# Kernel tuning notes

Hardware: AMD Instinct MI355X
Metric: run time of the kernel (lower is better)

Reference implementation:

```python
import jax, jax.numpy as jnp
import numpy as np

N_NODES = 100000

def _sage(x, src, tgt, Wl, bl, Wr):
    # PyG SAGEConv (mean aggr): out = lin_l(mean_{j in N(i)} x_j) + lin_r(x_i)
    msg = x[src]                                             # [E, F] gather
    s = jax.ops.segment_sum(msg, tgt, num_segments=N_NODES)  # [N, F]
    cnt = jax.ops.segment_sum(jnp.ones((src.shape[0], 1), x.dtype), tgt, num_segments=N_NODES)
    agg = s / jnp.maximum(cnt, 1.0)
    return agg @ Wl + bl + x @ Wr


def setup_inputs() -> dict:
    key = jax.random.key(0)
    ks = jax.random.split(key, 16)
    node_dim, edge_dim, hidden = 128, 16, 64
    E = 1000000
    x = jax.random.normal(ks[0], (N_NODES, node_dim), jnp.float32)
    edge_index = jax.random.randint(ks[1], (2, E), 0, N_NODES, jnp.int64)
    edge_attr = jax.random.normal(ks[2], (E, edge_dim), jnp.float32)
    def lin(k, fi, fo, scale=None):
        s = scale if scale is not None else 1.0 / np.sqrt(fi)
        return jax.random.uniform(k, (fi, fo), jnp.float32, -s, s)
    return {
        "x": x, "edge_index": edge_index, "edge_attr": edge_attr,
        # edge MLP: Linear(16,64) -> ReLU -> Linear(64,64)
        "We1": lin(ks[3], edge_dim, hidden), "be1": jnp.zeros((hidden,), jnp.float32),
        "We2": lin(ks[4], hidden, hidden),   "be2": jnp.zeros((hidden,), jnp.float32),
        # SAGEConv 0: lin_l (with bias, on aggregated) + lin_r (no bias, on root)
        "Wl0": lin(ks[5], node_dim, hidden), "bl0": jnp.zeros((hidden,), jnp.float32),
        "Wr0": lin(ks[6], node_dim, hidden),
        # SAGEConv 1
        "Wl1": lin(ks[7], hidden, hidden), "bl1": jnp.zeros((hidden,), jnp.float32),
        "Wr1": lin(ks[8], hidden, hidden),
        # output MLP: Linear(64,64) -> ReLU -> (Dropout eval=id) -> Linear(64,1)
        "Wo1": lin(ks[9], hidden, hidden), "bo1": jnp.zeros((hidden,), jnp.float32),
        "Wo2": lin(ks[10], hidden, 1),     "bo2": jnp.zeros((1,), jnp.float32),
    }


def reference(x, edge_index, edge_attr, We1, be1, We2, be2,
              Wl0, bl0, Wr0, Wl1, bl1, Wr1, Wo1, bo1, Wo2, bo2):
    src, tgt = edge_index[0], edge_index[1]
    # edge MLP (dropout in eval mode = identity)
    ea = jax.nn.relu(edge_attr @ We1 + be1) @ We2 + be2       # [E, H]
    # two SAGE layers with ReLU
    h = jax.nn.relu(_sage(x, src, tgt, Wl0, bl0, Wr0))        # [N, H]
    h = jax.nn.relu(_sage(h, src, tgt, Wl1, bl1, Wr1))        # [N, H]
    # per-edge features: gather both endpoints + edge embedding
    ef = h[src] + h[tgt] + ea                                 # [E, H]
    out = jax.nn.relu(ef @ Wo1 + bo1) @ Wo2 + bo2             # [E, 1]
    return jax.nn.sigmoid(out[:, 0])                          # [E]
```

## Files before the change

kernel.cpp:

```cpp
#include <hip/hip_runtime.h>
#include <math.h>

typedef __attribute__((ext_vector_type(8))) short short8;
typedef __attribute__((ext_vector_type(4))) float f32x4;

#define CAPB 4096

static __device__ __forceinline__ unsigned short f2bf(float f) {
  union { float f; unsigned int u; } x; x.f = f;
  unsigned int r = x.u + 0x7fffu + ((x.u >> 16) & 1u);
  return (unsigned short)(r >> 16);
}
static __device__ __forceinline__ float bf2f(unsigned int u) {
  union { unsigned int u; float f; } x; x.u = u << 16; return x.f;
}

__global__ void k_flag(const unsigned int* __restrict__ w, int nSample,
                       unsigned int* __restrict__ flag,
                       int* __restrict__ gcursor) {
  if (blockIdx.x == 1) {
    if (threadIdx.x < 256) { gcursor[threadIdx.x] = 0; gcursor[threadIdx.x + 256] = 0; }
    return;
  }
  if (blockIdx.x != 0) return;
  __shared__ unsigned int red[256];
  unsigned int v = 0;
  for (int i = threadIdx.x; i < nSample; i += 256) v |= w[2 * i + 1];
  red[threadIdx.x] = v;
  __syncthreads();
  for (int s = 128; s > 0; s >>= 1) {
    if (threadIdx.x < s) red[threadIdx.x] |= red[threadIdx.x + s];
    __syncthreads();
  }
  if (threadIdx.x == 0) flag[0] = red[0];
}

template <int K, bool BF16IN, int NTILES, bool INLINEW>
__device__ __forceinline__ void ngemm_body(
    const void* __restrict__ Xv, const unsigned short* __restrict__ WnT,
    const float* __restrict__ W0f, const float* __restrict__ W1f,
    unsigned short* __restrict__ Y0, unsigned short* __restrict__ Y1,
    int N, int blk, unsigned short* __restrict__ sX) {
  constexpr int STR = K + 8;
  constexpr int NC = K / 32;
  const int tid = threadIdx.x;
  const int wv = tid >> 6, lane = tid & 63;
  const int m = lane & 15, q = lane >> 4;
  const int row0 = blk * 64;

  short8 bB[NTILES][NC];
#pragma unroll
  for (int ct = 0; ct < NTILES; ++ct)
#pragma unroll
    for (int c = 0; c < NC; ++c) {
      if constexpr (INLINEW) {
        int n = (NTILES == 2) ? (wv * 32 + ct * 16 + m) : (wv * 16 + m);
        const float* Wf = (n < 64) ? W0f : W1f;
        int nn = n & 63;
        union { short8 s; unsigned short h[8]; } ub;
#pragma unroll
        for (int j = 0; j < 8; ++j)
          ub.h[j] = f2bf(Wf[(size_t)(c * 32 + q * 8 + j) * 64 + nn]);
        bB[ct][c] = ub.s;
      } else {
        int n = (NTILES == 2) ? (wv * 32 + ct * 16 + m) : (wv * 16 + m);
        bB[ct][c] = *(const short8*)(WnT + (size_t)n * K + c * 32 + q * 8);
      }
    }

#pragma unroll
  for (int i = 0; i < K / 16; ++i) {
    int f = tid + 256 * i;
    int r = f / (K / 4);
    int c4 = f % (K / 4);
    int rr = row0 + r; if (rr >= N) rr = N - 1;
    uint2 pk;
    if constexpr (BF16IN) {
      pk = *(const uint2*)((const unsigned short*)Xv + (size_t)rr * K + c4 * 4);
    } else {
      float4 v = *(const float4*)((const float*)Xv + (size_t)rr * K + c4 * 4);
      pk.x = (unsigned int)f2bf(v.x) | ((unsigned int)f2bf(v.y) << 16);
      pk.y = (unsigned int)f2bf(v.z) | ((unsigned int)f2bf(v.w) << 16);
    }
    *(uint2*)(sX + r * STR + c4 * 4) = pk;
  }
  __syncthreads();

  f32x4 acc[4][NTILES];
#pragma unroll
  for (int rt = 0; rt < 4; ++rt)
#pragma unroll
    for (int ct = 0; ct < NTILES; ++ct)
#pragma unroll
      for (int r = 0; r < 4; ++r) acc[rt][ct][r] = 0.f;

#pragma unroll
  for (int c = 0; c < NC; ++c) {
    short8 a[4];
#pragma unroll
    for (int rt = 0; rt < 4; ++rt)
      a[rt] = *(const short8*)(sX + (rt * 16 + m) * STR + c * 32 + q * 8);
#pragma unroll
    for (int rt = 0; rt < 4; ++rt)
#pragma unroll
      for (int ct = 0; ct < NTILES; ++ct)
        acc[rt][ct] = __builtin_amdgcn_mfma_f32_16x16x32_bf16(a[rt], bB[ct][c], acc[rt][ct], 0, 0, 0);
  }

#pragma unroll
  for (int rt = 0; rt < 4; ++rt)
#pragma unroll
    for (int ct = 0; ct < NTILES; ++ct) {
      unsigned short* Yw;
      int n;
      if constexpr (NTILES == 2) {
        Yw = (wv < 2) ? Y0 : Y1;
        n = (wv & 1) * 32 + ct * 16 + m;
      } else {
        Yw = Y0;
        n = wv * 16 + m;
      }
#pragma unroll
      for (int reg = 0; reg < 4; ++reg) {
        int row = row0 + rt * 16 + q * 4 + reg;
        if (row < N) Yw[(size_t)row * 64 + n] = f2bf(acc[rt][ct][reg]);
      }
    }
}

template <int K, bool BF16IN, int NTILES>
__global__ __launch_bounds__(256) void k_ngemm(
    const void* __restrict__ Xv, const unsigned short* __restrict__ WnT,
    unsigned short* __restrict__ Y0, unsigned short* __restrict__ Y1, int N) {
  __shared__ __align__(16) unsigned short sX[64 * (K + 8)];
  ngemm_body<K, BF16IN, NTILES, false>(Xv, WnT, nullptr, nullptr, Y0, Y1, N,
                                       blockIdx.x, sX);
}

__global__ __launch_bounds__(256) void k_mega1(
    const unsigned int* __restrict__ w, const unsigned int* __restrict__ flag,
    int E, int nDec, int nWork, int gB, int nConvThreads,
    int* __restrict__ src, int* __restrict__ tgt,
    int* __restrict__ gcursor, unsigned int* __restrict__ tmp,
    const float* __restrict__ x, unsigned short* __restrict__ Yl,
    unsigned short* __restrict__ Yr, int N,
    const float* __restrict__ We2, const float* __restrict__ Wo1,
    const float* __restrict__ be2, const float* __restrict__ bo1,
    const float* __restrict__ We1,
    const float* __restrict__ Wl0, const float* __restrict__ Wr0,
    const float* __restrict__ Wl1, const float* __restrict__ Wr1,
    unsigned short* __restrict__ W25T, unsigned short* __restrict__ We1T,
    unsigned short* __restrict__ Wo1T, float* __restrict__ cvec,
    unsigned short* __restrict__ WnT1,
    const float4* __restrict__ ef, uint2* __restrict__ eb) {
  __shared__ __align__(16) char smem[64 * 136 * 2];
  const int tid = threadIdx.x;
  const int tot = nDec + nWork;
  const int di  = (int)(((long long)blockIdx.x * nDec) / tot);
  const int di1 = (int)(((long long)(blockIdx.x + 1) * nDec) / tot);

  if (di1 > di) {
    int* hist = (int*)smem;
    hist[tid] = 0; hist[tid + 256] = 0;
    __syncthreads();
    const int e0 = di * 4096;
    const int e1 = (e0 + 4096 < E) ? (e0 + 4096) : E;
    const unsigned int fl = flag[0];
    for (int e = e0 + tid; e < e1; e += 256) {
      int s, t;
      if (fl) { s = (int)w[e]; t = (int)w[E + e]; }
      else    { s = (int)w[2 * e]; t = (int)w[2 * (E + e)]; }
      src[e] = s; tgt[e] = t;
      atomicAdd(hist + (t >> 8), 1);
    }
    __syncthreads();
    {
      int c0 = hist[tid], c1 = hist[tid + 256];
      int s0 = (c0 > 0) ? atomicAdd(gcursor + tid, c0) : 0;
      int s1 = (c1 > 0) ? atomicAdd(gcursor + tid + 256, c1) : 0;
      __syncthreads();
      hist[tid] = s0; hist[tid + 256] = s1;
    }
    __syncthreads();
    for (int e = e0 + tid; e < e1; e += 256) {
      int s, t;
      if (fl) { s = (int)w[e]; t = (int)w[E + e]; }
      else    { s = (int)w[2 * e]; t = (int)w[2 * (E + e)]; }
      int b = t >> 8;
      int pos = atomicAdd(hist + b, 1);
      if (pos < CAPB)
        tmp[(size_t)b * CAPB + pos] = ((unsigned int)s << 8) | (unsigned int)(t & 255);
    }
    return;
  }
  const int wi = blockIdx.x - di;
  if (wi == 0) {
    float* sB = (float*)smem;
    for (int i = tid; i < 1024; i += 256)
      *(float4*)&sB[i * 4] = *(const float4*)(Wo1 + i * 4);
    __syncthreads();
    for (int idx = tid; idx < 4096; idx += 256) {
      int k = idx >> 6, n = idx & 63;
      float s = 0.f;
#pragma unroll 8
      for (int mm = 0; mm < 64; ++mm) s = fmaf(We2[k * 64 + mm], sB[mm * 64 + n], s);
      W25T[n * 64 + k] = f2bf(s);
      Wo1T[n * 64 + k] = f2bf(sB[k * 64 + n]);
    }
    for (int idx = tid; idx < 2048; idx += 256) {
      int n = idx >> 5, k = idx & 31;
      We1T[n * 32 + k] = (k < 16) ? f2bf(We1[k * 64 + n]) : (unsigned short)0;
    }
    if (tid < 64) {
      float s = bo1[tid];
#pragma unroll 8
      for (int mm = 0; mm < 64; ++mm) s = fmaf(be2[mm], sB[mm * 64 + tid], s);
      cvec[tid] = s;
    }
  } else if (wi <= 32) {
    int idx = (wi - 1) * 256 + tid;
    int n = idx >> 6, k = idx & 63;
    float v = (n < 64) ? Wl1[(size_t)k * 64 + n] : Wr1[(size_t)k * 64 + (n - 64)];
    WnT1[idx] = f2bf(v);
  } else if (wi < 33 + gB) {
    ngemm_body<128, false, 2, true>(x, nullptr, Wl0, Wr0, Yl, Yr, N,
                                    wi - 33, (unsigned short*)smem);
  } else {
    int gid = (wi - 33 - gB) * 256 + tid;
    int nItems = E * 4;
    for (int i = gid; i < nItems; i += nConvThreads) {
      float4 v = ef[i];
      uint2 pk;
      pk.x = (unsigned int)f2bf(v.x) | ((unsigned int)f2bf(v.y) << 16);
      pk.y = (unsigned int)f2bf(v.z) | ((unsigned int)f2bf(v.w) << 16);
      eb[i] = pk;
    }
  }
}

__global__ __launch_bounds__(256) void k_bsort(
    const unsigned int* __restrict__ tmp, const int* __restrict__ gcursor,
    int* __restrict__ csrc, uint2* __restrict__ rowptr2, int N) {
  __shared__ int cnt[256];
  __shared__ int curs[256];
  __shared__ int wsum[4];
  const int b = blockIdx.x, tid = threadIdx.x;
  int c = gcursor[b]; if (c > CAPB) c = CAPB;
  cnt[tid] = 0;
  __syncthreads();
  const unsigned int* reg = tmp + (size_t)b * CAPB;
  for (int i = tid; i < c; i += 256) atomicAdd(&cnt[reg[i] & 255u], 1);
  __syncthreads();
  const int lane = tid & 63, wv = tid >> 6;
  int v = cnt[tid];
  int incl = v;
#pragma unroll
  for (int off = 1; off < 64; off <<= 1) {
    int t = __shfl_up(incl, off, 64);
    if (lane >= off) incl += t;
  }
  if (lane == 63) wsum[wv] = incl;
  __syncthreads();
  int add = 0;
  for (int ww = 0; ww < wv; ++ww) add += wsum[ww];
  int excl = add + incl - v;
  curs[tid] = excl;
  int node = b * 256 + tid;
  if (node < N)
    rowptr2[node] = make_uint2((unsigned int)(b * CAPB + excl),
                               (unsigned int)(b * CAPB + excl + v));
  __syncthreads();
  for (int i = tid; i < c; i += 256) {
    unsigned int wd = reg[i];
    int p = atomicAdd(&curs[wd & 255u], 1);
    csrc[(size_t)b * CAPB + p] = (int)(wd >> 8);
  }
}

__global__ __launch_bounds__(256) void k_agg(
    const unsigned short* __restrict__ Y, const uint2* __restrict__ rowptr2,
    const int* __restrict__ csrc, const float* __restrict__ bias,
    const unsigned short* __restrict__ Yr, unsigned short* __restrict__ H,
    int N) {
  int node = (blockIdx.x * 256 + threadIdx.x) >> 6;
  if (node >= N) return;
  const int lane = threadIdx.x & 63;
  const int c4 = lane & 15, rr = lane >> 4;
  uint2 be = rowptr2[node];
  int beg = (int)be.x, end = (int)be.y;
  float a0 = 0.f, a1 = 0.f, a2 = 0.f, a3 = 0.f;
  float b0 = 0.f, b1 = 0.f, b2 = 0.f, b3 = 0.f;
  for (int e = beg; e < end; e += 8) {
    int e0 = e + rr, e1 = e + 4 + rr;
    if (e0 < end) {
      int s = csrc[e0];
      uint2 v = *(const uint2*)(Y + (size_t)s * 64 + c4 * 4);
      a0 += bf2f(v.x & 0xffffu); a1 += bf2f(v.x >> 16);
      a2 += bf2f(v.y & 0xffffu); a3 += bf2f(v.y >> 16);
    }
    if (e1 < end) {
      int s = csrc[e1];
      uint2 v = *(const uint2*)(Y + (size_t)s * 64 + c4 * 4);
      b0 += bf2f(v.x & 0xffffu); b1 += bf2f(v.x >> 16);
      b2 += bf2f(v.y & 0xffffu); b3 += bf2f(v.y >> 16);
    }
  }
  a0 += b0; a1 += b1; a2 += b2; a3 += b3;
#pragma unroll
  for (int msk = 16; msk <= 32; msk <<= 1) {
    a0 += __shfl_xor(a0, msk, 64);
    a1 += __shfl_xor(a1, msk, 64);
    a2 += __shfl_xor(a2, msk, 64);
    a3 += __shfl_xor(a3, msk, 64);
  }
  if (rr == 0) {
    float cdeg = (float)(end - beg);
    if (cdeg < 1.f) cdeg = 1.f;
    float inv = 1.f / cdeg;
    float4 bv = *(const float4*)(bias + c4 * 4);
    uint2 yv = *(const uint2*)(Yr + (size_t)node * 64 + c4 * 4);
    float o0 = fmaxf(a0 * inv + bv.x + bf2f(yv.x & 0xffffu), 0.f);
    float o1 = fmaxf(a1 * inv + bv.y + bf2f(yv.x >> 16), 0.f);
    float o2 = fmaxf(a2 * inv + bv.z + bf2f(yv.y & 0xffffu), 0.f);
    float o3 = fmaxf(a3 * inv + bv.w + bf2f(yv.y >> 16), 0.f);
    uint2 pk;
    pk.x = (unsigned int)f2bf(o0) | ((unsigned int)f2bf(o1) << 16);
    pk.y = (unsigned int)f2bf(o2) | ((unsigned int)f2bf(o3) << 16);
    *(uint2*)(H + (size_t)node * 64 + c4 * 4) = pk;
  }
}

#define T1_STRIDE 72
#define G_STRIDE 68
__global__ __launch_bounds__(256) void k_edge3(
    const unsigned short* __restrict__ EAb, const int* __restrict__ src,
    const int* __restrict__ tgt, const unsigned short* __restrict__ Gb,
    const unsigned short* __restrict__ We1T,
    const unsigned short* __restrict__ W25T,
    const float* __restrict__ cvec, const float* __restrict__ be1,
    const float* __restrict__ Wo2, const float* __restrict__ bo2,
    float* __restrict__ out, int E, int nT, int nWaves) {
  __shared__ unsigned short sT1a[4][16 * T1_STRIDE];
  __shared__ float sGa[4][16 * G_STRIDE];
  const int tid = threadIdx.x;
  const int wid = tid >> 6, lane = tid & 63;
  const int m = lane & 15, q = lane >> 4;
  unsigned short* sT1 = sT1a[wid];
  float* sG = sGa[wid];

  short8 bWe1[4], bW25[4][2];
  float cv[4], wo2v[4], be1v[4];
#pragma unroll
  for (int nt = 0; nt < 4; ++nt) {
    int n = nt * 16 + m;
    bWe1[nt] = *(const short8*)(We1T + n * 32 + q * 8);
    bW25[nt][0] = *(const short8*)(W25T + n * 64 + q * 8);
    bW25[nt][1] = *(const short8*)(W25T + n * 64 + 32 + q * 8);
    cv[nt] = cvec[n];
    wo2v[nt] = Wo2[n];
    be1v[nt] = be1[n];
  }
  const float b_out = bo2[0];
  const short8 zfrag = {};

  int t = blockIdx.x * 4 + wid;
  if (t >= nT) return;
  int il = t * 16 + m; if (il >= E) il = E - 1;
  int my_idx = (lane < 16) ? src[il] : ((lane < 32) ? tgt[il] : 0);

  while (true) {
    const int base = t * 16;
    const int tn = t + nWaves;
    const bool last = (tn >= nT);
    const int tc = last ? t : tn;

    int il_n = tc * 16 + m; if (il_n >= E) il_n = E - 1;
    int idx_n = (lane < 16) ? src[il_n] : ((lane < 32) ? tgt[il_n] : 0);

    int rs[4], rt[4];
#pragma unroll
    for (int r = 0; r < 4; ++r) {
      rs[r] = __shfl(my_idx, q * 4 + r, 64);
      rt[r] = __shfl(my_idx, 16 + q * 4 + r, 64);
    }
    uint2 sv[4], tv[4];
#pragma unroll
    for (int r = 0; r < 4; ++r) {
      sv[r] = *(const uint2*)(Gb + (size_t)rs[r] * 64 + m * 4);
      tv[r] = *(const uint2*)(Gb + (size_t)rt[r] * 64 + m * 4);
    }

    int er = base + m; if (er >= E) er = E - 1;
    short8 aEA = zfrag;
    if (q < 2) aEA = *(const short8*)(EAb + (size_t)er * 16 + (q & 1) * 8);

    f32x4 t1[4];
#pragma unroll
    for (int nt = 0; nt < 4; ++nt) {
      f32x4 cinit; cinit[0] = be1v[nt]; cinit[1] = be1v[nt];
      cinit[2] = be1v[nt]; cinit[3] = be1v[nt];
      t1[nt] = __builtin_amdgcn_mfma_f32_16x16x32_bf16(aEA, bWe1[nt], cinit, 0, 0, 0);
    }
#pragma unroll
    for (int nt = 0; nt < 4; ++nt)
#pragma unroll
      for (int r = 0; r < 4; ++r)
        sT1[(q * 4 + r) * T1_STRIDE + nt * 16 + m] = f2bf(fmaxf(t1[nt][r], 0.f));
    short8 aT0 = *(short8*)(sT1 + m * T1_STRIDE + q * 8);
    short8 aT1 = *(short8*)(sT1 + m * T1_STRIDE + 32 + q * 8);

#pragma unroll
    for (int r = 0; r < 4; ++r) {
      f32x4 g;
      g[0] = bf2f(sv[r].x & 0xffffu) + bf2f(tv[r].x & 0xffffu);
      g[1] = bf2f(sv[r].x >> 16)     + bf2f(tv[r].x >> 16);
      g[2] = bf2f(sv[r].y & 0xffffu) + bf2f(tv[r].y & 0xffffu);
      g[3] = bf2f(sv[r].y >> 16)     + bf2f(tv[r].y >> 16);
      *(f32x4*)(sG + (q * 4 + r) * G_STRIDE + m * 4) = g;
    }

    f32x4 acc[4];
#pragma unroll
    for (int nt = 0; nt < 4; ++nt)
#pragma unroll
      for (int r = 0; r < 4; ++r)
        acc[nt][r] = cv[nt] + sG[(q * 4 + r) * G_STRIDE + nt * 16 + m];
#pragma unroll
    for (int nt = 0; nt < 4; ++nt) {
      acc[nt] = __builtin_amdgcn_mfma_f32_16x16x32_bf16(aT0, bW25[nt][0], acc[nt], 0, 0, 0);
      acc[nt] = __builtin_amdgcn_mfma_f32_16x16x32_bf16(aT1, bW25[nt][1], acc[nt], 0, 0, 0);
    }

    float p[4];
#pragma unroll
    for (int r = 0; r < 4; ++r) {
      p[r] = fmaxf(acc[0][r], 0.f) * wo2v[0] + fmaxf(acc[1][r], 0.f) * wo2v[1] +
             fmaxf(acc[2][r], 0.f) * wo2v[2] + fmaxf(acc[3][r], 0.f) * wo2v[3];
    }
#pragma unroll
    for (int msk = 1; msk <= 8; msk <<= 1) {
#pragma unroll
      for (int r = 0; r < 4; ++r) p[r] += __shfl_xor(p[r], msk, 64);
    }
    if (m == 0) {
#pragma unroll
      for (int r = 0; r < 4; ++r) {
        int row = base + q * 4 + r;
        if (row < E) out[row] = 1.f / (1.f + __expf(-(p[r] + b_out)));
      }
    }

    if (last) break;
    t = tn; my_idx = idx_n;
  }
}

extern "C" void kernel_launch(void* const* d_in, const int* in_sizes, int n_in,
                              void* d_out, int out_size, void* d_ws, size_t ws_size,
                              hipStream_t stream) {
  const float* x     = (const float*)d_in[0];
  const unsigned int* eidx = (const unsigned int*)d_in[1];
  const float* eattr = (const float*)d_in[2];
  const float* We1 = (const float*)d_in[3];
  const float* be1 = (const float*)d_in[4];
  const float* We2 = (const float*)d_in[5];
  const float* be2 = (const float*)d_in[6];
  const float* Wl0 = (const float*)d_in[7];
  const float* bl0 = (const float*)d_in[8];
  const float* Wr0 = (const float*)d_in[9];
  const float* Wl1 = (const float*)d_in[10];
  const float* bl1 = (const float*)d_in[11];
  const float* Wr1 = (const float*)d_in[12];
  const float* Wo1 = (const float*)d_in[13];
  const float* bo1 = (const float*)d_in[14];
  const float* Wo2 = (const float*)d_in[15];
  const float* bo2 = (const float*)d_in[16];

  const int N = in_sizes[0] / 128;
  const int E = in_sizes[2] / 16;
  const int NBUCK = (N + 255) >> 8;
  float* out = (float*)d_out;

  char* ws = (char*)d_ws;
  size_t off = 0;
  auto alloc = [&](size_t bytes) {
    char* p = ws + off;
    off += (bytes + 255) & ~(size_t)255;
    return p;
  };
  unsigned int* flag = (unsigned int*)alloc(256);
  int* src    = (int*)alloc((size_t)E * 4);
  int* tgt    = (int*)alloc((size_t)E * 4);
  int* gcursor = (int*)alloc(512 * 4);
  unsigned int* tmp = (unsigned int*)alloc((size_t)NBUCK * CAPB * 4);
  int* csrc   = (int*)alloc((size_t)NBUCK * CAPB * 4);
  uint2* rowptr2 = (uint2*)alloc((size_t)N * 8);
  unsigned short* EAb = (unsigned short*)alloc((size_t)E * 16 * 2);
  unsigned short* Hb = (unsigned short*)alloc((size_t)N * 64 * 2);
  unsigned short* Yl = (unsigned short*)alloc((size_t)N * 64 * 2);
  unsigned short* Yr = (unsigned short*)alloc((size_t)N * 64 * 2);
  unsigned short* Gb = (unsigned short*)alloc((size_t)N * 64 * 2);
  unsigned short* W25T = (unsigned short*)alloc(64 * 64 * 2);
  unsigned short* We1T = (unsigned short*)alloc(64 * 32 * 2);
  unsigned short* Wo1T = (unsigned short*)alloc(64 * 64 * 2);
  unsigned short* WnT1 = (unsigned short*)alloc(128 * 64 * 2);
  float* cvec = (float*)alloc(64 * 4);
  (void)ws_size; (void)n_in; (void)out_size;

  k_flag<<<2, 256, 0, stream>>>(eidx, 8192, flag, gcursor);

  const int nDec = (E + 4095) / 4096;
  const int gB = (N + 63) / 64;
  const int convB = 1024;
  const int nWork = 33 + gB + convB;
  k_mega1<<<nDec + nWork, 256, 0, stream>>>(
      eidx, flag, E, nDec, nWork, gB, convB * 256,
      src, tgt, gcursor, tmp,
      x, Yl, Yr, N,
      We2, Wo1, be2, bo1, We1, Wl0, Wr0, Wl1, Wr1,
      W25T, We1T, Wo1T, cvec, WnT1,
      (const float4*)eattr, (uint2*)EAb);

  k_bsort<<<NBUCK, 256, 0, stream>>>(tmp, gcursor, csrc, rowptr2, N);

  const int aggB = (N + 3) / 4;
  k_agg<<<aggB, 256, 0, stream>>>(Yl, rowptr2, csrc, bl0, Yr, Hb, N);

  k_ngemm<64, true, 2><<<gB, 256, 0, stream>>>(Hb, WnT1, Yl, Yr, N);
  k_agg<<<aggB, 256, 0, stream>>>(Yl, rowptr2, csrc, bl1, Yr, Hb, N);

  k_ngemm<64, true, 1><<<gB, 256, 0, stream>>>(Hb, Wo1T, Gb, nullptr, N);

  const int nT = (E + 15) / 16;
  const int blocks = 3072;
  k_edge3<<<blocks, 256, 0, stream>>>(EAb, src, tgt, Gb, We1T, W25T, cvec,
                                      be1, Wo2, bo2, out, E, nT, blocks * 4);
}
```

Before: 398.6 us.

## Replace global bucket cursor atomics with per-decode-block bucket slots

The edge bucketing pass no longer reserves space in each bucket with global atomicAdd on a shared cursor array. Each decode block now writes its per-bucket counts to a counts matrix and scatters into its own fixed-capacity slot region (48 entries per bucket per block). The bucket-sort kernel then scans all slots of each bucket, masked by those counts. This removes global atomic contention and the cursor reset from k_flag, at the cost of a sparser tmp layout, extra slot scanning and an integer division per slot. With one million edges over 391 buckets and 245 decode blocks, the expected per-slot load is about 16, so overflow past 48 is unlikely but would silently drop edges.

```diff
diff --git a/kernel.cpp b/kernel.cpp
--- a/kernel.cpp
+++ b/kernel.cpp
@@ -5,6 +5,8 @@
 typedef __attribute__((ext_vector_type(4))) float f32x4;
 
 #define CAPB 4096
+#define CAPPB 48
+#define NDECP 256
 
 static __device__ __forceinline__ unsigned short f2bf(float f) {
   union { float f; unsigned int u; } x; x.f = f;
@@ -16,13 +18,7 @@
 }
 
 __global__ void k_flag(const unsigned int* __restrict__ w, int nSample,
-                       unsigned int* __restrict__ flag,
-                       int* __restrict__ gcursor) {
-  if (blockIdx.x == 1) {
-    if (threadIdx.x < 256) { gcursor[threadIdx.x] = 0; gcursor[threadIdx.x + 256] = 0; }
-    return;
-  }
-  if (blockIdx.x != 0) return;
+                       unsigned int* __restrict__ flag) {
   __shared__ unsigned int red[256];
   unsigned int v = 0;
   for (int i = threadIdx.x; i < nSample; i += 256) v |= w[2 * i + 1];
@@ -141,7 +137,7 @@
     const unsigned int* __restrict__ w, const unsigned int* __restrict__ flag,
     int E, int nDec, int nWork, int gB, int nConvThreads,
     int* __restrict__ src, int* __restrict__ tgt,
-    int* __restrict__ gcursor, unsigned int* __restrict__ tmp,
+    int* __restrict__ counts, unsigned int* __restrict__ tmp,
     const float* __restrict__ x, unsigned short* __restrict__ Yl,
     unsigned short* __restrict__ Yr, int N,
     const float* __restrict__ We2, const float* __restrict__ Wo1,
@@ -176,10 +172,10 @@
     __syncthreads();
     {
       int c0 = hist[tid], c1 = hist[tid + 256];
-      int s0 = (c0 > 0) ? atomicAdd(gcursor + tid, c0) : 0;
-      int s1 = (c1 > 0) ? atomicAdd(gcursor + tid + 256, c1) : 0;
+      counts[(size_t)tid * NDECP + di] = c0;
+      counts[(size_t)(tid + 256) * NDECP + di] = c1;
       __syncthreads();
-      hist[tid] = s0; hist[tid + 256] = s1;
+      hist[tid] = 0; hist[tid + 256] = 0;
     }
     __syncthreads();
     for (int e = e0 + tid; e < e1; e += 256) {
@@ -188,8 +184,9 @@
       else    { s = (int)w[2 * e]; t = (int)w[2 * (E + e)]; }
       int b = t >> 8;
       int pos = atomicAdd(hist + b, 1);
-      if (pos < CAPB)
-        tmp[(size_t)b * CAPB + pos] = ((unsigned int)s << 8) | (unsigned int)(t & 255);
+      if (pos < CAPPB)
+        tmp[((size_t)b * NDECP + di) * CAPPB + pos] =
+            ((unsigned int)s << 8) | (unsigned int)(t & 255);
     }
     return;
   }
@@ -239,17 +236,22 @@
 }
 
 __global__ __launch_bounds__(256) void k_bsort(
-    const unsigned int* __restrict__ tmp, const int* __restrict__ gcursor,
-    int* __restrict__ csrc, uint2* __restrict__ rowptr2, int N) {
+    const unsigned int* __restrict__ tmp, const int* __restrict__ counts,
+    int* __restrict__ csrc, uint2* __restrict__ rowptr2, int N, int nDec) {
   __shared__ int cnt[256];
   __shared__ int curs[256];
   __shared__ int wsum[4];
+  __shared__ int scnt[NDECP];
   const int b = blockIdx.x, tid = threadIdx.x;
-  int c = gcursor[b]; if (c > CAPB) c = CAPB;
+  scnt[tid] = (tid < nDec) ? counts[(size_t)b * NDECP + tid] : 0;
   cnt[tid] = 0;
   __syncthreads();
-  const unsigned int* reg = tmp + (size_t)b * CAPB;
-  for (int i = tid; i < c; i += 256) atomicAdd(&cnt[reg[i] & 255u], 1);
+  const unsigned int* reg = tmp + (size_t)b * NDECP * CAPPB;
+  const int nSlots = nDec * CAPPB;
+  for (int idx = tid; idx < nSlots; idx += 256) {
+    int blk = idx / CAPPB, j = idx - blk * CAPPB;
+    if (j < scnt[blk]) atomicAdd(&cnt[reg[idx] & 255u], 1);
+  }
   __syncthreads();
   const int lane = tid & 63, wv = tid >> 6;
   int v = cnt[tid];
@@ -270,10 +272,13 @@
     rowptr2[node] = make_uint2((unsigned int)(b * CAPB + excl),
                                (unsigned int)(b * CAPB + excl + v));
   __syncthreads();
-  for (int i = tid; i < c; i += 256) {
-    unsigned int wd = reg[i];
-    int p = atomicAdd(&curs[wd & 255u], 1);
-    csrc[(size_t)b * CAPB + p] = (int)(wd >> 8);
+  for (int idx = tid; idx < nSlots; idx += 256) {
+    int blk = idx / CAPPB, j = idx - blk * CAPPB;
+    if (j < scnt[blk]) {
+      unsigned int wd = reg[idx];
+      int p = atomicAdd(&curs[wd & 255u], 1);
+      csrc[(size_t)b * CAPB + p] = (int)(wd >> 8);
+    }
   }
 }
 
@@ -491,8 +496,8 @@
   unsigned int* flag = (unsigned int*)alloc(256);
   int* src    = (int*)alloc((size_t)E * 4);
   int* tgt    = (int*)alloc((size_t)E * 4);
-  int* gcursor = (int*)alloc(512 * 4);
-  unsigned int* tmp = (unsigned int*)alloc((size_t)NBUCK * CAPB * 4);
+  int* counts = (int*)alloc((size_t)512 * NDECP * 4);
+  unsigned int* tmp = (unsigned int*)alloc((size_t)NBUCK * NDECP * CAPPB * 4);
   int* csrc   = (int*)alloc((size_t)NBUCK * CAPB * 4);
   uint2* rowptr2 = (uint2*)alloc((size_t)N * 8);
   unsigned short* EAb = (unsigned short*)alloc((size_t)E * 16 * 2);
@@ -507,7 +512,7 @@
   float* cvec = (float*)alloc(64 * 4);
   (void)ws_size; (void)n_in; (void)out_size;
 
-  k_flag<<<2, 256, 0, stream>>>(eidx, 8192, flag, gcursor);
+  k_flag<<<1, 256, 0, stream>>>(eidx, 8192, flag);
 
   const int nDec = (E + 4095) / 4096;
   const int gB = (N + 63) / 64;
@@ -515,13 +520,13 @@
   const int nWork = 33 + gB + convB;
   k_mega1<<<nDec + nWork, 256, 0, stream>>>(
       eidx, flag, E, nDec, nWork, gB, convB * 256,
-      src, tgt, gcursor, tmp,
+      src, tgt, counts, tmp,
       x, Yl, Yr, N,
       We2, Wo1, be2, bo1, We1, Wl0, Wr0, Wl1, Wr1,
       W25T, We1T, Wo1T, cvec, WnT1,
       (const float4*)eattr, (uint2*)EAb);
 
-  k_bsort<<<NBUCK, 256, 0, stream>>>(tmp, gcursor, csrc, rowptr2, N);
+  k_bsort<<<NBUCK, 256, 0, stream>>>(tmp, counts, csrc, rowptr2, N, nDec);
 
   const int aggB = (N + 3) / 4;
   k_agg<<<aggB, 256, 0, stream>>>(Yl, rowptr2, csrc, bl0, Yr, Hb, N);
```

New measurement: 429.6 us. 1.08x slower.

## Pre-transpose layer-0 weights, reorder mega kernel blocks, prefetch gathered rows in edge loop

Applied to the files above, without the earlier changes.

The layer-0 SAGE weights are now converted to transposed bf16 in a small pre-kernel, which also takes over the flag/cursor setup and the layer-1 weight conversion. This replaces per-block strided fp32 weight loads inside the node GEMM. The mega kernel now puts the node-GEMM blocks first, halves the edge chunk per decode block, and gives each conversion block a fixed share instead of a grid-stride loop. The edge kernel prefetches the next tile's gathered Gb rows one iteration ahead and shares one LDS buffer between its two scratch arrays, at the cost of more registers in flight.

```diff
diff --git a/kernel.cpp b/kernel.cpp
--- a/kernel.cpp
+++ b/kernel.cpp
@@ -15,30 +15,42 @@
   union { unsigned int u; float f; } x; x.u = u << 16; return x.f;
 }
 
-__global__ void k_flag(const unsigned int* __restrict__ w, int nSample,
-                       unsigned int* __restrict__ flag,
-                       int* __restrict__ gcursor) {
-  if (blockIdx.x == 1) {
-    if (threadIdx.x < 256) { gcursor[threadIdx.x] = 0; gcursor[threadIdx.x + 256] = 0; }
-    return;
-  }
-  if (blockIdx.x != 0) return;
-  __shared__ unsigned int red[256];
-  unsigned int v = 0;
-  for (int i = threadIdx.x; i < nSample; i += 256) v |= w[2 * i + 1];
-  red[threadIdx.x] = v;
-  __syncthreads();
-  for (int s = 128; s > 0; s >>= 1) {
-    if (threadIdx.x < s) red[threadIdx.x] |= red[threadIdx.x + s];
+__global__ __launch_bounds__(256) void k_pre(
+    const unsigned int* __restrict__ w, int nSample,
+    unsigned int* __restrict__ flag, int* __restrict__ gcursor,
+    const float* __restrict__ Wl0, const float* __restrict__ Wr0,
+    const float* __restrict__ Wl1, const float* __restrict__ Wr1,
+    unsigned short* __restrict__ WnT1, unsigned short* __restrict__ WnT0) {
+  const int tid = threadIdx.x;
+  const int b = blockIdx.x;
+  if (b == 0) {
+    gcursor[tid] = 0; gcursor[tid + 256] = 0;
+    __shared__ unsigned int red[256];
+    unsigned int v = 0;
+    for (int i = tid; i < nSample; i += 256) v |= w[2 * i + 1];
+    red[tid] = v;
     __syncthreads();
-  }
-  if (threadIdx.x == 0) flag[0] = red[0];
-}
-
-template <int K, bool BF16IN, int NTILES, bool INLINEW>
+    for (int s = 128; s > 0; s >>= 1) {
+      if (tid < s) red[tid] |= red[tid + s];
+      __syncthreads();
+    }
+    if (tid == 0) flag[0] = red[0];
+  } else if (b <= 32) {
+    int idx = (b - 1) * 256 + tid;
+    int n = idx >> 6, k = idx & 63;
+    float v = (n < 64) ? Wl1[(size_t)k * 64 + n] : Wr1[(size_t)k * 64 + (n - 64)];
+    WnT1[idx] = f2bf(v);
+  } else {
+    int idx = (b - 33) * 256 + tid;
+    int n = idx >> 7, k = idx & 127;
+    float v = (n < 64) ? Wl0[(size_t)k * 64 + n] : Wr0[(size_t)k * 64 + (n - 64)];
+    WnT0[idx] = f2bf(v);
+  }
+}
+
+template <int K, bool BF16IN, int NTILES>
 __device__ __forceinline__ void ngemm_body(
     const void* __restrict__ Xv, const unsigned short* __restrict__ WnT,
-    const float* __restrict__ W0f, const float* __restrict__ W1f,
     unsigned short* __restrict__ Y0, unsigned short* __restrict__ Y1,
     int N, int blk, unsigned short* __restrict__ sX) {
   constexpr int STR = K + 8;
@@ -53,19 +65,8 @@
   for (int ct = 0; ct < NTILES; ++ct)
 #pragma unroll
     for (int c = 0; c < NC; ++c) {
-      if constexpr (INLINEW) {
-        int n = (NTILES == 2) ? (wv * 32 + ct * 16 + m) : (wv * 16 + m);
-        const float* Wf = (n < 64) ? W0f : W1f;
-        int nn = n & 63;
-        union { short8 s; unsigned short h[8]; } ub;
-#pragma unroll
-        for (int j = 0; j < 8; ++j)
-          ub.h[j] = f2bf(Wf[(size_t)(c * 32 + q * 8 + j) * 64 + nn]);
-        bB[ct][c] = ub.s;
-      } else {
-        int n = (NTILES == 2) ? (wv * 32 + ct * 16 + m) : (wv * 16 + m);
-        bB[ct][c] = *(const short8*)(WnT + (size_t)n * K + c * 32 + q * 8);
-      }
+      int n = (NTILES == 2) ? (wv * 32 + ct * 16 + m) : (wv * 16 + m);
+      bB[ct][c] = *(const short8*)(WnT + (size_t)n * K + c * 32 + q * 8);
     }
 
 #pragma unroll
@@ -133,38 +134,37 @@
     const void* __restrict__ Xv, const unsigned short* __restrict__ WnT,
     unsigned short* __restrict__ Y0, unsigned short* __restrict__ Y1, int N) {
   __shared__ __align__(16) unsigned short sX[64 * (K + 8)];
-  ngemm_body<K, BF16IN, NTILES, false>(Xv, WnT, nullptr, nullptr, Y0, Y1, N,
-                                       blockIdx.x, sX);
+  ngemm_body<K, BF16IN, NTILES>(Xv, WnT, Y0, Y1, N, blockIdx.x, sX);
 }
 
 __global__ __launch_bounds__(256) void k_mega1(
     const unsigned int* __restrict__ w, const unsigned int* __restrict__ flag,
-    int E, int nDec, int nWork, int gB, int nConvThreads,
+    int E, int nDec, int gB,
     int* __restrict__ src, int* __restrict__ tgt,
     int* __restrict__ gcursor, unsigned int* __restrict__ tmp,
-    const float* __restrict__ x, unsigned short* __restrict__ Yl,
-    unsigned short* __restrict__ Yr, int N,
+    const float* __restrict__ x, const unsigned short* __restrict__ WnT0,
+    unsigned short* __restrict__ Yl, unsigned short* __restrict__ Yr, int N,
     const float* __restrict__ We2, const float* __restrict__ Wo1,
     const float* __restrict__ be2, const float* __restrict__ bo1,
     const float* __restrict__ We1,
-    const float* __restrict__ Wl0, const float* __restrict__ Wr0,
-    const float* __restrict__ Wl1, const float* __restrict__ Wr1,
     unsigned short* __restrict__ W25T, unsigned short* __restrict__ We1T,
     unsigned short* __restrict__ Wo1T, float* __restrict__ cvec,
-    unsigned short* __restrict__ WnT1,
     const float4* __restrict__ ef, uint2* __restrict__ eb) {
   __shared__ __align__(16) char smem[64 * 136 * 2];
   const int tid = threadIdx.x;
-  const int tot = nDec + nWork;
-  const int di  = (int)(((long long)blockIdx.x * nDec) / tot);
-  const int di1 = (int)(((long long)(blockIdx.x + 1) * nDec) / tot);
-
-  if (di1 > di) {
+  const int wi = blockIdx.x;
+
+  if (wi < gB) {
+    ngemm_body<128, false, 2>(x, WnT0, Yl, Yr, N, wi, (unsigned short*)smem);
+    return;
+  }
+  if (wi < gB + nDec) {
+    const int di = wi - gB;
     int* hist = (int*)smem;
     hist[tid] = 0; hist[tid + 256] = 0;
     __syncthreads();
-    const int e0 = di * 4096;
-    const int e1 = (e0 + 4096 < E) ? (e0 + 4096) : E;
+    const int e0 = di * 2048;
+    const int e1 = (e0 + 2048 < E) ? (e0 + 2048) : E;
     const unsigned int fl = flag[0];
     for (int e = e0 + tid; e < e1; e += 256) {
       int s, t;
@@ -193,8 +193,7 @@
     }
     return;
   }
-  const int wi = blockIdx.x - di;
-  if (wi == 0) {
+  if (wi == gB + nDec) {
     float* sB = (float*)smem;
     for (int i = tid; i < 1024; i += 256)
       *(float4*)&sB[i * 4] = *(const float4*)(Wo1 + i * 4);
@@ -217,18 +216,14 @@
       for (int mm = 0; mm < 64; ++mm) s = fmaf(be2[mm], sB[mm * 64 + tid], s);
       cvec[tid] = s;
     }
-  } else if (wi <= 32) {
-    int idx = (wi - 1) * 256 + tid;
-    int n = idx >> 6, k = idx & 63;
-    float v = (n < 64) ? Wl1[(size_t)k * 64 + n] : Wr1[(size_t)k * 64 + (n - 64)];
-    WnT1[idx] = f2bf(v);
-  } else if (wi < 33 + gB) {
-    ngemm_body<128, false, 2, true>(x, nullptr, Wl0, Wr0, Yl, Yr, N,
-                                    wi - 33, (unsigned short*)smem);
-  } else {
-    int gid = (wi - 33 - gB) * 256 + tid;
-    int nItems = E * 4;
-    for (int i = gid; i < nItems; i += nConvThreads) {
+    return;
+  }
+  const int ci = wi - (gB + nDec + 1);
+  const int nItems = E * 4;
+#pragma unroll
+  for (int j = 0; j < 4; ++j) {
+    int i = ci * 1024 + j * 256 + tid;
+    if (i < nItems) {
       float4 v = ef[i];
       uint2 pk;
       pk.x = (unsigned int)f2bf(v.x) | ((unsigned int)f2bf(v.y) << 16);
@@ -340,13 +335,12 @@
     const float* __restrict__ cvec, const float* __restrict__ be1,
     const float* __restrict__ Wo2, const float* __restrict__ bo2,
     float* __restrict__ out, int E, int nT, int nWaves) {
-  __shared__ unsigned short sT1a[4][16 * T1_STRIDE];
-  __shared__ float sGa[4][16 * G_STRIDE];
+  __shared__ __align__(16) char sBuf[4][4352];
   const int tid = threadIdx.x;
   const int wid = tid >> 6, lane = tid & 63;
   const int m = lane & 15, q = lane >> 4;
-  unsigned short* sT1 = sT1a[wid];
-  float* sG = sGa[wid];
+  unsigned short* sT1 = (unsigned short*)sBuf[wid];
+  float* sG = (float*)sBuf[wid];
 
   short8 bWe1[4], bW25[4][2];
   float cv[4], wo2v[4], be1v[4];
@@ -365,8 +359,19 @@
 
   int t = blockIdx.x * 4 + wid;
   if (t >= nT) return;
-  int il = t * 16 + m; if (il >= E) il = E - 1;
-  int my_idx = (lane < 16) ? src[il] : ((lane < 32) ? tgt[il] : 0);
+
+  uint2 sv[4], tv[4];
+  {
+    int il = t * 16 + m; if (il >= E) il = E - 1;
+    int my = (lane < 16) ? src[il] : ((lane < 32) ? tgt[il] : 0);
+#pragma unroll
+    for (int r = 0; r < 4; ++r) {
+      int a = __shfl(my, q * 4 + r, 64);
+      int b = __shfl(my, 16 + q * 4 + r, 64);
+      sv[r] = *(const uint2*)(Gb + (size_t)a * 64 + m * 4);
+      tv[r] = *(const uint2*)(Gb + (size_t)b * 64 + m * 4);
+    }
+  }
 
   while (true) {
     const int base = t * 16;
@@ -376,18 +381,13 @@
 
     int il_n = tc * 16 + m; if (il_n >= E) il_n = E - 1;
     int idx_n = (lane < 16) ? src[il_n] : ((lane < 32) ? tgt[il_n] : 0);
-
-    int rs[4], rt[4];
+    uint2 sv_n[4], tv_n[4];
 #pragma unroll
     for (int r = 0; r < 4; ++r) {
-      rs[r] = __shfl(my_idx, q * 4 + r, 64);
-      rt[r] = __shfl(my_idx, 16 + q * 4 + r, 64);
-    }
-    uint2 sv[4], tv[4];
-#pragma unroll
-    for (int r = 0; r < 4; ++r) {
-      sv[r] = *(const uint2*)(Gb + (size_t)rs[r] * 64 + m * 4);
-      tv[r] = *(const uint2*)(Gb + (size_t)rt[r] * 64 + m * 4);
+      int a = __shfl(idx_n, q * 4 + r, 64);
+      int b = __shfl(idx_n, 16 + q * 4 + r, 64);
+      sv_n[r] = *(const uint2*)(Gb + (size_t)a * 64 + m * 4);
+      tv_n[r] = *(const uint2*)(Gb + (size_t)b * 64 + m * 4);
     }
 
     int er = base + m; if (er >= E) er = E - 1;
@@ -451,7 +451,9 @@
     }
 
     if (last) break;
-    t = tn; my_idx = idx_n;
+    t = tn;
+#pragma unroll
+    for (int r = 0; r < 4; ++r) { sv[r] = sv_n[r]; tv[r] = tv_n[r]; }
   }
 }
 
@@ -504,21 +506,23 @@
   unsigned short* We1T = (unsigned short*)alloc(64 * 32 * 2);
   unsigned short* Wo1T = (unsigned short*)alloc(64 * 64 * 2);
   unsigned short* WnT1 = (unsigned short*)alloc(128 * 64 * 2);
+  unsigned short* WnT0 = (unsigned short*)alloc(128 * 128 * 2);
   float* cvec = (float*)alloc(64 * 4);
   (void)ws_size; (void)n_in; (void)out_size;
 
-  k_flag<<<2, 256, 0, stream>>>(eidx, 8192, flag, gcursor);
-
-  const int nDec = (E + 4095) / 4096;
+  const int nDec = (E + 2047) / 2048;
   const int gB = (N + 63) / 64;
-  const int convB = 1024;
-  const int nWork = 33 + gB + convB;
-  k_mega1<<<nDec + nWork, 256, 0, stream>>>(
-      eidx, flag, E, nDec, nWork, gB, convB * 256,
+  const int nConv = (E * 4 + 1023) / 1024;
+
+  k_pre<<<97, 256, 0, stream>>>(eidx, 8192, flag, gcursor,
+                                Wl0, Wr0, Wl1, Wr1, WnT1, WnT0);
+
+  k_mega1<<<gB + nDec + 1 + nConv, 256, 0, stream>>>(
+      eidx, flag, E, nDec, gB,
       src, tgt, gcursor, tmp,
-      x, Yl, Yr, N,
-      We2, Wo1, be2, bo1, We1, Wl0, Wr0, Wl1, Wr1,
-      W25T, We1T, Wo1T, cvec, WnT1,
+      x, WnT0, Yl, Yr, N,
+      We2, Wo1, be2, bo1, We1,
+      W25T, We1T, Wo1T, cvec,
       (const float4*)eattr, (uint2*)EAb);
 
   k_bsort<<<NBUCK, 256, 0, stream>>>(tmp, gcursor, csrc, rowptr2, N);
```

Result: slower. 429.6 us (+7.8%).
